# Kernel tuning notes

Hardware: AMD Instinct MI355X
Metric: run time of the kernel (lower is better)

## Reference

```python
import jax, jax.numpy as jnp
import numpy as np

N, C, H, W = 32, 512, 32, 32
S = 2048
INFLUENCE = 1.0  # influence_decay='constant', training_progress irrelevant


def setup_inputs() -> dict:
    key = jax.random.key(0)
    k1, k2 = jax.random.split(key)
    x = jax.random.normal(k1, (N, C, H, W), dtype=jnp.float32)
    # nn.Parameter(torch.randn(S, C) / C)
    codebook = jax.random.normal(k2, (S, C), dtype=jnp.float32) / C
    return {"x": x, "codebook": codebook}


def _distances(x_flat, codebook):
    # x_flat: [N, C, P], codebook: [S, C] -> [N, S, P]
    # same math as ((x[:,None]-cb[None,...,None])**2).sum(2), without the
    # [N, S, C, P] intermediate
    x2 = jnp.sum(x_flat * x_flat, axis=1)          # [N, P]
    c2 = jnp.sum(codebook * codebook, axis=1)      # [S]
    xc = jnp.einsum('ncp,sc->nsp', x_flat, codebook)  # [N, S, P]
    return x2[:, None, :] + c2[None, :, None] - 2.0 * xc


def reference(x, codebook):
    n, c = x.shape[:2]
    x_flat = x.reshape(n, c, -1)                      # [N, C, P]
    xs = jax.lax.stop_gradient(x_flat)                # distance(x_flat.detach())
    d = _distances(xs, codebook)                      # [N, S, P]
    idx = jnp.argmin(d, axis=1)                       # [N, P]
    xq = jnp.transpose(codebook[idx], (0, 2, 1)).reshape(x.shape)  # [N,C,H,W]
    loss_commitment = jnp.mean((x - jax.lax.stop_gradient(xq)) ** 2)
    d_sorted = jnp.sort(d, axis=1)                    # ascending over S
    w = jnp.exp(-jnp.arange(d.shape[1], dtype=jnp.float32) / INFLUENCE)
    loss_codebook = jnp.mean(w[None, :, None] * d_sorted)
    codebook_indices = idx.reshape(n, *x.shape[2:])   # [N, H, W]
    output = x + jax.lax.stop_gradient(xq - x)        # straight-through
    return (loss_codebook, loss_commitment, codebook_indices, output)
```

## Files before the change

### kernel.cpp

```cpp
#include <hip/hip_runtime.h>
#include <hip/hip_fp16.h>

#define N_ 32
#define C_ 512
#define P_ 1024
#define S_ 2048
#define NR_ (N_ * P_)
#define GUARD 6e-3f
#define TSIG 2.3f

typedef __attribute__((ext_vector_type(8))) short sh8;
typedef __attribute__((ext_vector_type(4))) float fx4;

#define WS_XT       0ull
#define WS_XTF      33554432ull
#define WS_CBT      100663296ull
#define WS_C2F      102760448ull
#define WS_X2       102768640ull
#define WS_CNT      102899712ull
#define WS_CANDV    103030784ull
#define WS_CANDS    111419392ull
#define WS_ROWPART  119808000ull
#define WS_COMMIT   120070144ull
#define WS_TOTAL    120201216ull

#define TBLK 1024
#define CVTBLK 512

__device__ __forceinline__ unsigned short f2bf(float f) {
  union { float f; unsigned u; } x; x.f = f;
  unsigned r = x.u + 0x7fffu + ((x.u >> 16) & 1u);
  return (unsigned short)(r >> 16);
}

template <typename T>
__device__ __forceinline__ void load16_lds(const T* g, T* l) {
  __builtin_amdgcn_global_load_lds((const __attribute__((address_space(1))) void*)g,
                                   (__attribute__((address_space(3))) void*)l, 16, 0, 0);
}

__global__ __launch_bounds__(256) void k_prep(const float* __restrict__ x,
                                              const float* __restrict__ cb,
                                              unsigned short* __restrict__ xT,
                                              float* __restrict__ xTf,
                                              unsigned short* __restrict__ cbT,
                                              float* __restrict__ c2f,
                                              float* __restrict__ x2ws,
                                              int* __restrict__ cnt) {
  __shared__ float tile[32][260];
  const int tid = threadIdx.x;
  const int bx = blockIdx.x;

  if (bx < TBLK) {
    const int n = bx >> 5;
    const int p0 = (bx & 31) << 5;
    const float* xb = x + (size_t)n * (C_ * P_) + p0;
    const int p4 = (tid & 7) << 2;
    const int ch = tid >> 3;

    float acc = 0.f;
#pragma unroll
    for (int pass = 0; pass < 2; ++pass) {
      if (pass) __syncthreads();
#pragma unroll
      for (int it = 0; it < 8; ++it) {
        int cl = (it << 5) + ch;
        float4 v = *(const float4*)(xb + (size_t)(pass * 256 + cl) * P_ + p4);
        tile[p4 + 0][cl] = v.x;
        tile[p4 + 1][cl] = v.y;
        tile[p4 + 2][cl] = v.z;
        tile[p4 + 3][cl] = v.w;
      }
      __syncthreads();

#pragma unroll
      for (int it = 0; it < 8; ++it) {
        int idx = tid + 256 * it;
        int row = idx >> 6, c4 = (idx & 63) << 2;
        float4 f = *(const float4*)&tile[row][c4];
        size_t R = (size_t)((n << 10) + p0 + row);
        size_t cg = (size_t)pass * 256 + c4;
        *(float4*)(xTf + R * C_ + cg) = f;
        ushort4 o;
        o.x = f2bf(f.x); o.y = f2bf(f.y); o.z = f2bf(f.z); o.w = f2bf(f.w);
        *(ushort4*)(xT + R * C_ + cg) = o;
      }

      if (tid < 32) {
        for (int c = 0; c < 256; ++c) {
          float t = tile[tid][c];
          acc = __fadd_rn(acc, __fmul_rn(t, t));
        }
      }
    }
    if (tid < 32) {
      int R = (n << 10) + p0 + tid;
      x2ws[R] = acc;
      cnt[R] = 0;
    }
  } else {
    const int s = (bx - TBLK) * 4 + (tid >> 6);
    const int l = tid & 63;
    const float* row = cb + (size_t)s * C_;
    double c2d = 0.0;
#pragma unroll
    for (int h = 0; h < 2; ++h) {
      int c = h * 256 + l * 4;
      float4 v = *(const float4*)(row + c);
      ushort4 o;
      o.x = f2bf(v.x); o.y = f2bf(v.y); o.z = f2bf(v.z); o.w = f2bf(v.w);
      *(ushort4*)(cbT + (size_t)s * C_ + c) = o;
      c2d += (double)__fmul_rn(v.x, v.x) + (double)__fmul_rn(v.y, v.y) +
             (double)__fmul_rn(v.z, v.z) + (double)__fmul_rn(v.w, v.w);
    }
#pragma unroll
    for (int off = 32; off > 0; off >>= 1) c2d += __shfl_down(c2d, off);
    if (l == 0) c2f[s] = (float)c2d;
  }
}

__global__ __launch_bounds__(256, 4) void k_gemm(const unsigned short* __restrict__ xT,
                                                 const unsigned short* __restrict__ cbT,
                                                 const float* __restrict__ x2ws,
                                                 float* __restrict__ candv,
                                                 int* __restrict__ cands,
                                                 int* __restrict__ cnt) {
  __shared__ unsigned short As[128 * 64];
  __shared__ unsigned short Bs[128 * 64];
  __shared__ float t_lds[128];
  const int tid = threadIdx.x;
  const int w = tid >> 6, l = tid & 63;
  const int bx = blockIdx.x;
  const int m_tile = ((bx >> 7) << 3) + (bx & 7);
  const int s_tile = (bx >> 3) & 15;
  const int m0 = m_tile << 7, s0 = s_tile << 7;
  const int wm = (w & 1) << 6, wsf = (w >> 1) << 6;
  const int quad = l >> 4, lane15 = l & 15;

  if (tid < 128) t_lds[tid] = TSIG * __fsqrt_rn(x2ws[m0 + tid]) * (1.0f / 512.0f);

  size_t gA[4], gB[4];
  unsigned short *lA[4], *lB[4];
#pragma unroll
  for (int q = 0; q < 4; ++q) {
    int chunk = (q * 4 + w) * 64 + l;
    int m = chunk >> 3, k8s = chunk & 7;
    int k8 = k8s ^ (m & 7);
    gA[q] = (size_t)(m0 + m) * (C_ * 2) + (size_t)k8 * 16;
    gB[q] = (size_t)(s0 + m) * (C_ * 2) + (size_t)k8 * 16;
    lA[q] = As + (q * 4 + w) * 512;
    lB[q] = Bs + (q * 4 + w) * 512;
  }
  const char* xb = (const char*)xT;
  const char* cbb = (const char*)cbT;

  fx4 acc[4][4];
#pragma unroll
  for (int i = 0; i < 4; ++i)
#pragma unroll
    for (int j = 0; j < 4; ++j) acc[i][j] = (fx4){0.f, 0.f, 0.f, 0.f};

  for (int kk = 0; kk < 8; ++kk) {
#pragma unroll
    for (int q = 0; q < 4; ++q) {
      load16_lds((const unsigned short*)(xb + gA[q] + (size_t)kk * 128), lA[q]);
      load16_lds((const unsigned short*)(cbb + gB[q] + (size_t)kk * 128), lB[q]);
    }
    __syncthreads();
#pragma unroll
    for (int ks = 0; ks < 2; ++ks) {
      const int k8g = ks * 4 + quad;
      sh8 af[4], bf[4];
#pragma unroll
      for (int mi = 0; mi < 4; ++mi) {
        int m = wm + mi * 16 + lane15;
        af[mi] = *(const sh8*)(As + m * 64 + (k8g ^ (m & 7)) * 8);
      }
#pragma unroll
      for (int si = 0; si < 4; ++si) {
        int s = wsf + si * 16 + lane15;
        bf[si] = *(const sh8*)(Bs + s * 64 + (k8g ^ (s & 7)) * 8);
      }
#pragma unroll
      for (int mi = 0; mi < 4; ++mi)
#pragma unroll
        for (int si = 0; si < 4; ++si)
          acc[mi][si] = __builtin_amdgcn_mfma_f32_16x16x32_bf16(af[mi], bf[si], acc[mi][si], 0, 0, 0);
    }
    __syncthreads();
  }

  const unsigned below = (1u << lane15) - 1u;
#pragma unroll
  for (int mi = 0; mi < 4; ++mi) {
#pragma unroll
    for (int r = 0; r < 4; ++r) {
      const int rowl = wm + mi * 16 + quad * 4 + r;
      const int rowg = m0 + rowl;
      const float t = t_lds[rowl];
      float v[4]; int scol[4]; bool hit[4];
      float vmax = -1e30f; int smax = 0;
#pragma unroll
      for (int si = 0; si < 4; ++si) {
        v[si] = acc[mi][si][r];
        scol[si] = s0 + wsf + si * 16 + lane15;
        hit[si] = v[si] >= t;
        if (v[si] > vmax) { vmax = v[si]; smax = scol[si]; }
      }
      int total = 0, myslot[4];
#pragma unroll
      for (int si = 0; si < 4; ++si) {
        unsigned long long b = __ballot(hit[si]);
        unsigned seg = (unsigned)((b >> (quad * 16)) & 0xFFFFull);
        myslot[si] = total + __popc(seg & below);
        total += __popc(seg);
      }
#pragma unroll
      for (int off = 1; off < 16; off <<= 1) {
        float ov = __shfl_xor(vmax, off);
        int os = __shfl_xor(smax, off);
        if (ov > vmax) { vmax = ov; smax = os; }
      }
      int base = 0;
      if (lane15 == 0) base = atomicAdd(&cnt[rowg], total > 0 ? total : 1);
      base = __shfl(base, quad * 16);
      if (total > 0) {
#pragma unroll
        for (int si = 0; si < 4; ++si) {
          if (hit[si]) {
            int slot = base + myslot[si];
            if (slot < 64) {
              candv[(size_t)rowg * 64 + slot] = v[si];
              cands[(size_t)rowg * 64 + slot] = scol[si];
            }
          }
        }
      } else if (lane15 == 0 && base < 64) {
        candv[(size_t)rowg * 64 + base] = vmax;
        cands[(size_t)rowg * 64 + base] = smax;
      }
    }
  }
}

__global__ __launch_bounds__(256, 4) void k_phase2(
    const float* __restrict__ cb, const float* __restrict__ xTf,
    const float* __restrict__ candvG, const int* __restrict__ candsG,
    const int* __restrict__ cntG, const float* __restrict__ c2f,
    const float* __restrict__ x2ws, float* __restrict__ out,
    double* __restrict__ rowpart) {
  __shared__ float xrow[4][C_];
  __shared__ float dt_l[4][64];
  __shared__ int s_l[4][64];
  __shared__ double cpart[4];
  const int tid = threadIdx.x;
  const int w = tid >> 6, l = tid & 63;
  const int R = blockIdx.x * 4 + w;

  const int cnt = min(cntG[R], 64);
  const float x2f = x2ws[R];
  const bool act = l < cnt;
  float v = candvG[(size_t)R * 64 + l];
  int s = candsG[(size_t)R * 64 + l];
  v = act ? v : -1e30f;
  s = act ? s : 0x7fffffff;
  const int sIdx = act ? s : 0;
  const float dt = act
      ? __fsub_rn(__fadd_rn(x2f, c2f[sIdx]), __fmul_rn(2.f, v))
      : 1e30f;

  float M = v;
#pragma unroll
  for (int off = 1; off < 64; off <<= 1) M = fmaxf(M, __shfl_xor(M, off));

  dt_l[w][l] = dt;
  s_l[w][l] = s;
  asm volatile("s_waitcnt lgkmcnt(0)" ::: "memory");

  int rank = 0;
#pragma unroll
  for (int k4 = 0; k4 < 16; ++k4) {
    float4 dk = *(const float4*)&dt_l[w][k4 * 4];
    int4 sk = *(const int4*)&s_l[w][k4 * 4];
    rank += (dk.x < dt || (dk.x == dt && sk.x < s)) ? 1 : 0;
    rank += (dk.y < dt || (dk.y == dt && sk.y < s)) ? 1 : 0;
    rank += (dk.z < dt || (dk.z == dt && sk.z < s)) ? 1 : 0;
    rank += (dk.w < dt || (dk.w == dt && sk.w < s)) ? 1 : 0;
  }

  double contrib = act ? (double)__expf(-(float)rank) * (double)dt : 0.0;
#pragma unroll
  for (int off = 32; off > 0; off >>= 1) contrib += __shfl_down(contrib, off);
  if (l == 0) cpart[w] = contrib;

  const bool near = act && (v >= M - GUARD);
  const unsigned long long bal = __ballot(near);
  const int nres = __popcll(bal);
  if (nres == 1) {
    int src = __ffsll(bal) - 1;
    int wins = __shfl(s, src);
    if (l == 0) out[2 + R] = (float)wins;
  } else {
#pragma unroll
    for (int k = 0; k < 2; ++k)
      *(float4*)&xrow[w][l * 8 + k * 4] = *(const float4*)(xTf + (size_t)R * C_ + l * 8 + k * 4);
    float d32 = 1e30f;
    if (near) {
      const float4* crow = (const float4*)(cb + (size_t)s * C_);
      float acc = 0.f;
#pragma unroll 8
      for (int i = 0; i < C_ / 4; ++i) {
        float4 cv = crow[i];
        float4 xv = *(const float4*)&xrow[w][i * 4];
        acc = __fadd_rn(acc, __fmul_rn(xv.x, cv.x));
        acc = __fadd_rn(acc, __fmul_rn(xv.y, cv.y));
        acc = __fadd_rn(acc, __fmul_rn(xv.z, cv.z));
        acc = __fadd_rn(acc, __fmul_rn(xv.w, cv.w));
      }
      d32 = __fsub_rn(__fadd_rn(x2f, c2f[s]), __fmul_rn(2.f, acc));
    }
    float bd = d32;
    int bs2 = near ? s : 0x7fffffff;
#pragma unroll
    for (int off = 1; off < 64; off <<= 1) {
      float ov = __shfl_xor(bd, off);
      int os = __shfl_xor(bs2, off);
      if (ov < bd || (ov == bd && os < bs2)) { bd = ov; bs2 = os; }
    }
    if (l == 0) out[2 + R] = (float)bs2;
  }

  __syncthreads();
  if (tid == 0) rowpart[blockIdx.x] = cpart[0] + cpart[1] + cpart[2] + cpart[3];
}

__global__ __launch_bounds__(512) void k2_output(
    const float* __restrict__ x, const float* __restrict__ cb,
    float* __restrict__ out, double* __restrict__ commit_partial) {
  __shared__ float qt[32][516];
  __shared__ int s_lds[32];
  __shared__ double r2[8];
  const int tid = threadIdx.x;
  const int bx = blockIdx.x;
  const int n = bx >> 5;
  const int p0 = (bx & 31) << 5;

  if (tid < 32) s_lds[tid] = (int)out[2 + n * P_ + p0 + tid];
  __syncthreads();
  {
    const int p = tid >> 4, c0 = (tid & 15) << 2;
    const float* row = cb + (size_t)s_lds[p] * C_;
#pragma unroll
    for (int it = 0; it < 8; ++it) {
      int c = c0 + (it << 6);
      *(float4*)&qt[p][c] = *(const float4*)(row + c);
    }
  }
  __syncthreads();

  const int cl = tid >> 3, pq = (tid & 7) << 2;
  double dacc = 0.0;
#pragma unroll
  for (int chunk = 0; chunk < 8; ++chunk) {
    int c = (chunk << 6) + cl;
    const float* xr = x + ((size_t)n * C_ + c) * P_ + p0 + pq;
    float4 xv = *(const float4*)xr;
    float xs[4] = {xv.x, xv.y, xv.z, xv.w};
    float o[4];
    float acc = 0.f;
#pragma unroll
    for (int k = 0; k < 4; ++k) {
      float q = qt[pq + k][c];
      float t = __fsub_rn(q, xs[k]);
      o[k] = __fadd_rn(xs[k], t);
      float dd = __fsub_rn(xs[k], q);
      acc += dd * dd;
    }
    float* orow = out + 2 + N_ * P_ + ((size_t)n * C_ + c) * P_ + p0 + pq;
    *(float4*)orow = make_float4(o[0], o[1], o[2], o[3]);
    dacc += (double)acc;
  }

#pragma unroll
  for (int off = 32; off > 0; off >>= 1) dacc += __shfl_down(dacc, off);
  if ((tid & 63) == 0) r2[tid >> 6] = dacc;
  __syncthreads();
  if (tid == 0) {
    double t = 0.0;
#pragma unroll
    for (int i = 0; i < 8; ++i) t += r2[i];
    commit_partial[bx] = t;
  }
}

__global__ __launch_bounds__(256) void k3_finalize(
    const double* __restrict__ pa, int na, const double* __restrict__ pb, int nb,
    float* __restrict__ out) {
  __shared__ double red[8];
  const int tid = threadIdx.x;
  double a = 0.0, b = 0.0;
  for (int i = tid; i < na; i += 256) a += pa[i];
  for (int i = tid; i < nb; i += 256) b += pb[i];
#pragma unroll
  for (int off = 32; off > 0; off >>= 1) {
    a += __shfl_down(a, off);
    b += __shfl_down(b, off);
  }
  if ((tid & 63) == 0) {
    red[(tid >> 6) * 2 + 0] = a;
    red[(tid >> 6) * 2 + 1] = b;
  }
  __syncthreads();
  if (tid == 0) {
    double A = red[0] + red[2] + red[4] + red[6];
    double B = red[1] + red[3] + red[5] + red[7];
    out[0] = (float)(A / ((double)N_ * (double)S_ * (double)P_));
    out[1] = (float)(B / ((double)N_ * (double)C_ * (double)P_));
  }
}

#define TPW 8
#define KC 32
#define SC 64
#define KCF 48
__global__ __launch_bounds__(256) void k1_fallback(
    const float* __restrict__ x, const float* __restrict__ cb,
    float* __restrict__ out, double* __restrict__ cb_partial) {
  __shared__ float dval[TPW][KCF];
  __shared__ float x2f[TPW];
  __shared__ double redd[4];
  __shared__ float x_t[TPW][C_ + 4];
  __shared__ float cb_t[SC][KC + 4];
  __shared__ int cand_s[TPW][KCF];
  __shared__ _Float16 sc[S_][TPW];

  const int tid = threadIdx.x;
  const int bx = blockIdx.x;
  const int n = bx >> 7;
  const int p0 = (bx & 127) * TPW;

  const float* xn = x + (size_t)n * C_ * P_ + p0;
#pragma unroll
  for (int q = 0; q < 16; ++q) {
    int e = tid + 256 * q;
    int c = e >> 3, j = e & 7;
    x_t[j][c] = xn[(size_t)c * P_ + j];
  }
  __syncthreads();
  if (tid < TPW) {
    float acc = 0.f;
    for (int c = 0; c < C_; ++c)
      acc = __fadd_rn(acc, __fmul_rn(x_t[tid][c], x_t[tid][c]));
    x2f[tid] = acc;
  }
  const int j = tid & 7;
  const int sg = tid >> 3;
  for (int s0 = 0; s0 < S_; s0 += SC) {
    float acc0 = 0.f, acc1 = 0.f;
    for (int k0 = 0; k0 < C_; k0 += KC) {
      __syncthreads();
#pragma unroll
      for (int q = 0; q < 8; ++q) {
        int e = tid + 256 * q;
        int i = e >> 5, cc = e & 31;
        cb_t[i][cc] = cb[(size_t)(s0 + i) * C_ + k0 + cc];
      }
      __syncthreads();
      const float* xr = &x_t[j][k0];
#pragma unroll
      for (int cs = 0; cs < KC; cs += 4) {
        float4 xv = *(const float4*)(xr + cs);
        float4 a4 = *(const float4*)(&cb_t[sg][cs]);
        float4 b4 = *(const float4*)(&cb_t[sg + 32][cs]);
        acc0 += xv.x * a4.x + xv.y * a4.y + xv.z * a4.z + xv.w * a4.w;
        acc1 += xv.x * b4.x + xv.y * b4.y + xv.z * b4.z + xv.w * b4.w;
      }
    }
    sc[s0 + sg][j] = (_Float16)acc0;
    sc[s0 + sg + 32][j] = (_Float16)acc1;
  }
  __syncthreads();
  {
    const int g = tid >> 5, t = tid & 31;
    for (int pass = 0; pass < KCF; ++pass) {
      float bv = -1e30f;
      int bs = 0;
      for (int k = 0; k < 64; ++k) {
        int s = t + 32 * k;
        float vv = (float)sc[s][g];
        if (vv > bv) { bv = vv; bs = s; }
      }
#pragma unroll
      for (int off = 1; off < 32; off <<= 1) {
        float ov = __shfl_xor(bv, off);
        int os = __shfl_xor(bs, off);
        if (ov > bv || (ov == bv && os < bs)) { bv = ov; bs = os; }
      }
      if (t == 0) {
        cand_s[g][pass] = bs;
        sc[bs][g] = (_Float16)(-65504.f);
      }
      __syncthreads();
    }
  }
  for (int task = tid; task < TPW * KCF; task += 256) {
    int jj = task / KCF, r = task % KCF;
    int s = cand_s[jj][r];
    const float* row = cb + (size_t)s * C_;
    const float* xrw = &x_t[jj][0];
    float acc = 0.f;
    double c2d = 0.0;
    for (int c = 0; c < C_; c += 4) {
      float4 cv = *(const float4*)(row + c);
      acc = __fadd_rn(acc, __fmul_rn(xrw[c + 0], cv.x));
      acc = __fadd_rn(acc, __fmul_rn(xrw[c + 1], cv.y));
      acc = __fadd_rn(acc, __fmul_rn(xrw[c + 2], cv.z));
      acc = __fadd_rn(acc, __fmul_rn(xrw[c + 3], cv.w));
      c2d += (double)__fmul_rn(cv.x, cv.x);
      c2d += (double)__fmul_rn(cv.y, cv.y);
      c2d += (double)__fmul_rn(cv.z, cv.z);
      c2d += (double)__fmul_rn(cv.w, cv.w);
    }
    float c2s = (float)c2d;
    dval[jj][r] = __fsub_rn(__fadd_rn(x2f[jj], c2s), __fmul_rn(2.f, acc));
  }
  __syncthreads();
  double contrib = 0.0;
  for (int task = tid; task < TPW * KCF; task += 256) {
    int jj = task / KCF, r = task % KCF;
    float e = dval[jj][r];
    int s = cand_s[jj][r];
    int rank = 0;
    for (int r2 = 0; r2 < KCF; ++r2) {
      float e2 = dval[jj][r2];
      int s2 = cand_s[jj][r2];
      rank += (e2 < e || (e2 == e && s2 < s)) ? 1 : 0;
    }
    contrib += exp((double)(-rank)) * (double)e;
    if (rank == 0) out[2 + n * P_ + p0 + jj] = (float)s;
  }
  __syncthreads();
#pragma unroll
  for (int off = 32; off > 0; off >>= 1) contrib += __shfl_down(contrib, off);
  if ((tid & 63) == 0) redd[tid >> 6] = contrib;
  __syncthreads();
  if (tid == 0) cb_partial[bx] = redd[0] + redd[1] + redd[2] + redd[3];
}

extern "C" void kernel_launch(void* const* d_in, const int* in_sizes, int n_in,
                              void* d_out, int out_size, void* d_ws, size_t ws_size,
                              hipStream_t stream) {
  const float* x = (const float*)d_in[0];
  const float* cb = (const float*)d_in[1];
  float* out = (float*)d_out;
  char* ws = (char*)d_ws;

  if (ws_size >= WS_TOTAL) {
    unsigned short* xT = (unsigned short*)(ws + WS_XT);
    float* xTf = (float*)(ws + WS_XTF);
    unsigned short* cbT = (unsigned short*)(ws + WS_CBT);
    float* c2f = (float*)(ws + WS_C2F);
    float* x2ws = (float*)(ws + WS_X2);
    int* cnt = (int*)(ws + WS_CNT);
    float* candv = (float*)(ws + WS_CANDV);
    int* cands = (int*)(ws + WS_CANDS);
    double* rowpart = (double*)(ws + WS_ROWPART);
    double* commitp = (double*)(ws + WS_COMMIT);

    hipLaunchKernelGGL(k_prep, dim3(TBLK + CVTBLK), dim3(256), 0, stream,
                       x, cb, xT, xTf, cbT, c2f, x2ws, cnt);
    hipLaunchKernelGGL(k_gemm, dim3(4096), dim3(256), 0, stream,
                       xT, cbT, x2ws, candv, cands, cnt);
    hipLaunchKernelGGL(k_phase2, dim3(NR_ / 4), dim3(256), 0, stream,
                       cb, xTf, candv, cands, cnt, c2f, x2ws, out, rowpart);
    hipLaunchKernelGGL(k2_output, dim3(1024), dim3(512), 0, stream, x, cb, out, commitp);
    hipLaunchKernelGGL(k3_finalize, dim3(1), dim3(256), 0, stream,
                       rowpart, NR_ / 4, commitp, 1024, out);
  } else {
    double* cb_partial = (double*)d_ws;
    double* commitp = cb_partial + 4096;
    hipLaunchKernelGGL(k1_fallback, dim3(4096), dim3(256), 0, stream, x, cb, out, cb_partial);
    hipLaunchKernelGGL(k2_output, dim3(1024), dim3(512), 0, stream, x, cb, out, commitp);
    hipLaunchKernelGGL(k3_finalize, dim3(1), dim3(256), 0, stream,
                       cb_partial, 4096, commitp, 1024, out);
  }
}
```

Before: 412.0 us.

## Fuse candidate resolution, output write and finalize into one tail kernel

Merges the phase-2 candidate resolution, the straight-through output/commitment kernel and the single-block finalize into one kernel. Each 512-thread block handles 32 pixels of one image, resolves their winners into shared memory, and then gathers the codebook rows directly. The final reduction runs in the last block to finish, found through an atomic counter that the prep kernel resets. This removes two kernel launches and the round trip of indices through global memory. In exchange there are fewer, larger blocks for the phase-2 work, and the result depends on a threadfence/atomic last-block pattern.

```diff
diff --git a/kernel.cpp b/kernel.cpp
--- a/kernel.cpp
+++ b/kernel.cpp
@@ -22,6 +22,7 @@
 #define WS_CANDS    111419392ull
 #define WS_ROWPART  119808000ull
 #define WS_COMMIT   120070144ull
+#define WS_DONE     (WS_COMMIT + 65536ull)
 #define WS_TOTAL    120201216ull
 
 #define TBLK 1024
@@ -46,12 +47,14 @@
                                               unsigned short* __restrict__ cbT,
                                               float* __restrict__ c2f,
                                               float* __restrict__ x2ws,
-                                              int* __restrict__ cnt) {
+                                              int* __restrict__ cnt,
+                                              int* __restrict__ done) {
   __shared__ float tile[32][260];
   const int tid = threadIdx.x;
   const int bx = blockIdx.x;
 
   if (bx < TBLK) {
+    if (bx == 0 && tid == 0) *done = 0;
     const int n = bx >> 5;
     const int p0 = (bx & 31) << 5;
     const float* xb = x + (size_t)n * (C_ * P_) + p0;
@@ -243,95 +246,178 @@
   }
 }
 
-__global__ __launch_bounds__(256, 4) void k_phase2(
+__global__ __launch_bounds__(512) void k_tail(
     const float* __restrict__ cb, const float* __restrict__ xTf,
     const float* __restrict__ candvG, const int* __restrict__ candsG,
     const int* __restrict__ cntG, const float* __restrict__ c2f,
-    const float* __restrict__ x2ws, float* __restrict__ out,
-    double* __restrict__ rowpart) {
-  __shared__ float xrow[4][C_];
-  __shared__ float dt_l[4][64];
-  __shared__ int s_l[4][64];
-  __shared__ double cpart[4];
+    const float* __restrict__ x2ws, const float* __restrict__ x,
+    float* __restrict__ out, double* __restrict__ rowpart,
+    double* __restrict__ commitp, int* __restrict__ done) {
+  __shared__ float smem[32 * 516];
+  __shared__ int win[32];
+  __shared__ double cpart[8];
+  __shared__ double r2[8];
+  __shared__ int lastF;
   const int tid = threadIdx.x;
-  const int w = tid >> 6, l = tid & 63;
-  const int R = blockIdx.x * 4 + w;
-
-  const int cnt = min(cntG[R], 64);
-  const float x2f = x2ws[R];
-  const bool act = l < cnt;
-  float v = candvG[(size_t)R * 64 + l];
-  int s = candsG[(size_t)R * 64 + l];
-  v = act ? v : -1e30f;
-  s = act ? s : 0x7fffffff;
-  const int sIdx = act ? s : 0;
-  const float dt = act
-      ? __fsub_rn(__fadd_rn(x2f, c2f[sIdx]), __fmul_rn(2.f, v))
-      : 1e30f;
-
-  float M = v;
-#pragma unroll
-  for (int off = 1; off < 64; off <<= 1) M = fmaxf(M, __shfl_xor(M, off));
-
-  dt_l[w][l] = dt;
-  s_l[w][l] = s;
-  asm volatile("s_waitcnt lgkmcnt(0)" ::: "memory");
-
-  int rank = 0;
-#pragma unroll
-  for (int k4 = 0; k4 < 16; ++k4) {
-    float4 dk = *(const float4*)&dt_l[w][k4 * 4];
-    int4 sk = *(const int4*)&s_l[w][k4 * 4];
-    rank += (dk.x < dt || (dk.x == dt && sk.x < s)) ? 1 : 0;
-    rank += (dk.y < dt || (dk.y == dt && sk.y < s)) ? 1 : 0;
-    rank += (dk.z < dt || (dk.z == dt && sk.z < s)) ? 1 : 0;
-    rank += (dk.w < dt || (dk.w == dt && sk.w < s)) ? 1 : 0;
-  }
-
-  double contrib = act ? (double)__expf(-(float)rank) * (double)dt : 0.0;
-#pragma unroll
-  for (int off = 32; off > 0; off >>= 1) contrib += __shfl_down(contrib, off);
-  if (l == 0) cpart[w] = contrib;
-
-  const bool near = act && (v >= M - GUARD);
-  const unsigned long long bal = __ballot(near);
-  const int nres = __popcll(bal);
-  if (nres == 1) {
-    int src = __ffsll(bal) - 1;
-    int wins = __shfl(s, src);
-    if (l == 0) out[2 + R] = (float)wins;
-  } else {
-#pragma unroll
-    for (int k = 0; k < 2; ++k)
-      *(float4*)&xrow[w][l * 8 + k * 4] = *(const float4*)(xTf + (size_t)R * C_ + l * 8 + k * 4);
-    float d32 = 1e30f;
-    if (near) {
-      const float4* crow = (const float4*)(cb + (size_t)s * C_);
-      float acc = 0.f;
+  const int wv = tid >> 6, l = tid & 63;
+  const int bx = blockIdx.x;
+  const int n = bx >> 5;
+  const int p0 = (bx & 31) << 5;
+
+  float* xrow_w = smem + wv * 512;
+  float* dt_w = smem + 8 * 512 + wv * 64;
+  int* s_w = (int*)(smem + 8 * 512 + 8 * 64) + wv * 64;
+
+  double contribAcc = 0.0;
+#pragma unroll
+  for (int j = 0; j < 4; ++j) {
+    const int pl = (j << 3) + wv;
+    const int R = (n << 10) + p0 + pl;
+    const int cnt = min(cntG[R], 64);
+    const float x2f = x2ws[R];
+    const bool act = l < cnt;
+    float v = candvG[(size_t)R * 64 + l];
+    int s = candsG[(size_t)R * 64 + l];
+    v = act ? v : -1e30f;
+    s = act ? s : 0x7fffffff;
+    const int sIdx = act ? s : 0;
+    const float dt = act
+        ? __fsub_rn(__fadd_rn(x2f, c2f[sIdx]), __fmul_rn(2.f, v))
+        : 1e30f;
+
+    float M = v;
+#pragma unroll
+    for (int off = 1; off < 64; off <<= 1) M = fmaxf(M, __shfl_xor(M, off));
+
+    dt_w[l] = dt;
+    s_w[l] = s;
+    asm volatile("s_waitcnt lgkmcnt(0)" ::: "memory");
+
+    int rank = 0;
+#pragma unroll
+    for (int k4 = 0; k4 < 16; ++k4) {
+      float4 dk = *(const float4*)&dt_w[k4 * 4];
+      int4 sk = *(const int4*)&s_w[k4 * 4];
+      rank += (dk.x < dt || (dk.x == dt && sk.x < s)) ? 1 : 0;
+      rank += (dk.y < dt || (dk.y == dt && sk.y < s)) ? 1 : 0;
+      rank += (dk.z < dt || (dk.z == dt && sk.z < s)) ? 1 : 0;
+      rank += (dk.w < dt || (dk.w == dt && sk.w < s)) ? 1 : 0;
+    }
+
+    double contrib = act ? (double)__expf(-(float)rank) * (double)dt : 0.0;
+#pragma unroll
+    for (int off = 32; off > 0; off >>= 1) contrib += __shfl_down(contrib, off);
+    if (l == 0) contribAcc += contrib;
+
+    const bool near = act && (v >= M - GUARD);
+    const unsigned long long bal = __ballot(near);
+    const int nres = __popcll(bal);
+    if (nres == 1) {
+      int src = __ffsll(bal) - 1;
+      int wins = __shfl(s, src);
+      if (l == 0) { win[pl] = wins; out[2 + R] = (float)wins; }
+    } else {
+#pragma unroll
+      for (int k = 0; k < 2; ++k)
+        *(float4*)&xrow_w[l * 8 + k * 4] = *(const float4*)(xTf + (size_t)R * C_ + l * 8 + k * 4);
+      float d32 = 1e30f;
+      if (near) {
+        const float4* crow = (const float4*)(cb + (size_t)s * C_);
+        float acc = 0.f;
 #pragma unroll 8
-      for (int i = 0; i < C_ / 4; ++i) {
-        float4 cv = crow[i];
-        float4 xv = *(const float4*)&xrow[w][i * 4];
-        acc = __fadd_rn(acc, __fmul_rn(xv.x, cv.x));
-        acc = __fadd_rn(acc, __fmul_rn(xv.y, cv.y));
-        acc = __fadd_rn(acc, __fmul_rn(xv.z, cv.z));
-        acc = __fadd_rn(acc, __fmul_rn(xv.w, cv.w));
-      }
-      d32 = __fsub_rn(__fadd_rn(x2f, c2f[s]), __fmul_rn(2.f, acc));
-    }
-    float bd = d32;
-    int bs2 = near ? s : 0x7fffffff;
-#pragma unroll
-    for (int off = 1; off < 64; off <<= 1) {
-      float ov = __shfl_xor(bd, off);
-      int os = __shfl_xor(bs2, off);
-      if (ov < bd || (ov == bd && os < bs2)) { bd = ov; bs2 = os; }
-    }
-    if (l == 0) out[2 + R] = (float)bs2;
-  }
-
-  __syncthreads();
-  if (tid == 0) rowpart[blockIdx.x] = cpart[0] + cpart[1] + cpart[2] + cpart[3];
+        for (int i = 0; i < C_ / 4; ++i) {
+          float4 cv = crow[i];
+          float4 xv = *(const float4*)&xrow_w[i * 4];
+          acc = __fadd_rn(acc, __fmul_rn(xv.x, cv.x));
+          acc = __fadd_rn(acc, __fmul_rn(xv.y, cv.y));
+          acc = __fadd_rn(acc, __fmul_rn(xv.z, cv.z));
+          acc = __fadd_rn(acc, __fmul_rn(xv.w, cv.w));
+        }
+        d32 = __fsub_rn(__fadd_rn(x2f, c2f[s]), __fmul_rn(2.f, acc));
+      }
+      float bd = d32;
+      int bs2 = near ? s : 0x7fffffff;
+#pragma unroll
+      for (int off = 1; off < 64; off <<= 1) {
+        float ov = __shfl_xor(bd, off);
+        int os = __shfl_xor(bs2, off);
+        if (ov < bd || (ov == bd && os < bs2)) { bd = ov; bs2 = os; }
+      }
+      if (l == 0) { win[pl] = bs2; out[2 + R] = (float)bs2; }
+    }
+  }
+  if (l == 0) cpart[wv] = contribAcc;
+  __syncthreads();
+
+  float (*qt)[516] = (float(*)[516])smem;
+  {
+    const int p = tid >> 4, c0 = (tid & 15) << 2;
+    const float* row = cb + (size_t)win[p] * C_;
+#pragma unroll
+    for (int it = 0; it < 8; ++it) {
+      int c = c0 + (it << 6);
+      *(float4*)&qt[p][c] = *(const float4*)(row + c);
+    }
+  }
+  __syncthreads();
+
+  const int cl = tid >> 3, pq = (tid & 7) << 2;
+  double dacc = 0.0;
+#pragma unroll
+  for (int chunk = 0; chunk < 8; ++chunk) {
+    int c = (chunk << 6) + cl;
+    const float* xr = x + ((size_t)n * C_ + c) * P_ + p0 + pq;
+    float4 xv = *(const float4*)xr;
+    float xs[4] = {xv.x, xv.y, xv.z, xv.w};
+    float o[4];
+    float acc = 0.f;
+#pragma unroll
+    for (int k = 0; k < 4; ++k) {
+      float q = qt[pq + k][c];
+      float t = __fsub_rn(q, xs[k]);
+      o[k] = __fadd_rn(xs[k], t);
+      float dd = __fsub_rn(xs[k], q);
+      acc += dd * dd;
+    }
+    float* orow = out + 2 + N_ * P_ + ((size_t)n * C_ + c) * P_ + p0 + pq;
+    *(float4*)orow = make_float4(o[0], o[1], o[2], o[3]);
+    dacc += (double)acc;
+  }
+
+#pragma unroll
+  for (int off = 32; off > 0; off >>= 1) dacc += __shfl_down(dacc, off);
+  if ((tid & 63) == 0) r2[tid >> 6] = dacc;
+  __syncthreads();
+  if (tid == 0) {
+    double t = 0.0, rp = 0.0;
+#pragma unroll
+    for (int i = 0; i < 8; ++i) { t += r2[i]; rp += cpart[i]; }
+    commitp[bx] = t;
+    rowpart[bx] = rp;
+  }
+
+  __threadfence();
+  if (tid == 0) lastF = (atomicAdd(done, 1) == (int)gridDim.x - 1) ? 1 : 0;
+  __syncthreads();
+  if (lastF) {
+    __threadfence();
+    double a = 0.0, b = 0.0;
+    for (int i = tid; i < 1024; i += 512) { a += rowpart[i]; b += commitp[i]; }
+#pragma unroll
+    for (int off = 32; off > 0; off >>= 1) {
+      a += __shfl_down(a, off);
+      b += __shfl_down(b, off);
+    }
+    if ((tid & 63) == 0) { r2[tid >> 6] = a; cpart[tid >> 6] = b; }
+    __syncthreads();
+    if (tid == 0) {
+      double A = 0.0, B = 0.0;
+#pragma unroll
+      for (int i = 0; i < 8; ++i) { A += r2[i]; B += cpart[i]; }
+      out[0] = (float)(A / ((double)N_ * (double)S_ * (double)P_));
+      out[1] = (float)(B / ((double)N_ * (double)C_ * (double)P_));
+    }
+  }
 }
 
 __global__ __launch_bounds__(512) void k2_output(
@@ -566,16 +652,15 @@
     int* cands = (int*)(ws + WS_CANDS);
     double* rowpart = (double*)(ws + WS_ROWPART);
     double* commitp = (double*)(ws + WS_COMMIT);
+    int* done = (int*)(ws + WS_DONE);
 
     hipLaunchKernelGGL(k_prep, dim3(TBLK + CVTBLK), dim3(256), 0, stream,
-                       x, cb, xT, xTf, cbT, c2f, x2ws, cnt);
+                       x, cb, xT, xTf, cbT, c2f, x2ws, cnt, done);
     hipLaunchKernelGGL(k_gemm, dim3(4096), dim3(256), 0, stream,
                        xT, cbT, x2ws, candv, cands, cnt);
-    hipLaunchKernelGGL(k_phase2, dim3(NR_ / 4), dim3(256), 0, stream,
-                       cb, xTf, candv, cands, cnt, c2f, x2ws, out, rowpart);
-    hipLaunchKernelGGL(k2_output, dim3(1024), dim3(512), 0, stream, x, cb, out, commitp);
-    hipLaunchKernelGGL(k3_finalize, dim3(1), dim3(256), 0, stream,
-                       rowpart, NR_ / 4, commitp, 1024, out);
+    hipLaunchKernelGGL(k_tail, dim3(1024), dim3(512), 0, stream,
+                       cb, xTf, candv, cands, cnt, c2f, x2ws, x,
+                       out, rowpart, commitp, done);
   } else {
     double* cb_partial = (double*)d_ws;
     double* commitp = cb_partial + 4096;
```

Result: slower. 749.9 us (+82.0%).
